# Kernel tuning notes

Measured on AMD Instinct MI355X. Metric: run time of the kernel, lower is better.

The kernel has to match this reference:

```python
import jax, jax.numpy as jnp
import numpy as np

B, D, N, K = 4, 256, 4096, 8192


def setup_inputs() -> dict:
    key = jax.random.key(0)
    kx, ke = jax.random.split(key)
    x = jax.random.normal(kx, (B, D, N), dtype=jnp.float32)
    e = jax.random.normal(ke, (K, D), dtype=jnp.float32)
    return {"x": x, "e": e}


def reference(x, e):
    # encode: cdist(x^T [B,N,D], e [K,D]) -> [B,N,K]; argmin over K.
    # sqrt is monotonic, so argmin of squared distance == argmin of cdist.
    xt = jnp.transpose(x, (0, 2, 1))                      # [B,N,D]
    x2 = jnp.sum(xt * xt, axis=-1, keepdims=True)         # [B,N,1]
    e2 = jnp.sum(e * e, axis=-1)                          # [K]
    d2 = x2 - 2.0 * jnp.einsum('bnd,kd->bnk', xt, e) + e2 # [B,N,K]
    codes = jnp.argmin(d2, axis=-1)                       # [B,N]
    # decode: embedding gather then transpose back to [B,D,N]
    quantized = e[codes]                                  # [B,N,D]
    return jnp.transpose(quantized, (0, 2, 1))            # [B,D,N]
```

## Files before the change

### kernel.cpp

```cpp
#include <hip/hip_runtime.h>
#include <stdint.h>

#define B_ 4
#define D_ 256
#define N_ 4096
#define K_ 8192
#define Q_ (B_*N_)

typedef __attribute__((ext_vector_type(8))) short bf16x8;
typedef __attribute__((ext_vector_type(8))) unsigned short u16x8;
typedef __attribute__((ext_vector_type(16))) float f32x16;

__device__ __forceinline__ unsigned short f32_to_bf16(float f) {
  unsigned u = __float_as_uint(f);
  unsigned r = 0x7FFFu + ((u >> 16) & 1u);
  return (unsigned short)((u + r) >> 16);
}
__device__ __forceinline__ float bf16_to_f32(unsigned short h) {
  return __uint_as_float(((unsigned)h) << 16);
}

__device__ __forceinline__ void gl_lds16(const void* g, void* l) {
  __builtin_amdgcn_global_load_lds(
      (const __attribute__((address_space(1))) unsigned int*)g,
      (__attribute__((address_space(3))) unsigned int*)l, 16, 0, 0);
}

__global__ void prep_x_kernel(const float* __restrict__ x,
                              unsigned short* __restrict__ xh,
                              unsigned short* __restrict__ xl) {
  __shared__ float tile[64][65];
  int b = blockIdx.z;
  int d0 = blockIdx.y * 64;
  int n0 = blockIdx.x * 64;
  int tid = threadIdx.x;

  int rr = tid >> 4;
  int rc = (tid & 15) * 4;
  const float* xp = x + ((size_t)b * D_ + d0) * N_ + n0;
#pragma unroll
  for (int p = 0; p < 4; ++p) {
    float4 v = *(const float4*)(xp + (size_t)(rr + 16 * p) * N_ + rc);
    tile[rr + 16 * p][rc + 0] = v.x;
    tile[rr + 16 * p][rc + 1] = v.y;
    tile[rr + 16 * p][rc + 2] = v.z;
    tile[rr + 16 * p][rc + 3] = v.w;
  }
  __syncthreads();

  int nr = tid >> 3;
  int dc = tid & 7;
#pragma unroll
  for (int p = 0; p < 2; ++p) {
    int nn = nr + 32 * p;
    u16x8 h8, l8;
#pragma unroll
    for (int j = 0; j < 8; ++j) {
      float v = tile[dc * 8 + j][nn];
      unsigned short h = f32_to_bf16(v);
      h8[j] = h;
      l8[j] = f32_to_bf16(v - bf16_to_f32(h));
    }
    size_t q = (size_t)b * N_ + n0 + nn;
    *(u16x8*)(xh + q * D_ + d0 + dc * 8) = h8;
    *(u16x8*)(xl + q * D_ + d0 + dc * 8) = l8;
  }
}

__global__ void prep_e_kernel(const float* __restrict__ e,
                              unsigned short* __restrict__ eh,
                              unsigned short* __restrict__ el,
                              float* __restrict__ e2h,
                              unsigned long long* __restrict__ keys) {
  int tid = threadIdx.x;
  int k = blockIdx.x * 8 + (tid >> 5);
  int d = (tid & 31) * 8;
  if (tid < 16) keys[(size_t)blockIdx.x * 16 + tid] = ~0ull;
  const float* ep = e + (size_t)k * D_ + d;
  float4 v0 = *(const float4*)(ep);
  float4 v1 = *(const float4*)(ep + 4);
  float vv[8] = {v0.x, v0.y, v0.z, v0.w, v1.x, v1.y, v1.z, v1.w};
  u16x8 h8, l8;
  float s = 0.f;
#pragma unroll
  for (int j = 0; j < 8; ++j) {
    unsigned short h = f32_to_bf16(vv[j]);
    h8[j] = h;
    l8[j] = f32_to_bf16(vv[j] - bf16_to_f32(h));
    s += vv[j] * vv[j];
  }
  *(u16x8*)(eh + (size_t)k * D_ + d) = h8;
  *(u16x8*)(el + (size_t)k * D_ + d) = l8;
#pragma unroll
  for (int off = 16; off > 0; off >>= 1) s += __shfl_xor(s, off, 64);
  if ((tid & 31) == 0) e2h[k] = 0.5f * s;
}

__global__ __launch_bounds__(256, 1) void vq_main_kernel(
    const unsigned short* __restrict__ xh, const unsigned short* __restrict__ xl,
    const unsigned short* __restrict__ eh, const unsigned short* __restrict__ el,
    const float* __restrict__ e2h, unsigned long long* __restrict__ keys) {
  __shared__ __attribute__((aligned(16))) unsigned short Bs[2][2][32 * 256];

  const int tid = threadIdx.x;
  const int w = tid >> 6;
  const int lane = tid & 63;
  const int l = lane & 31;
  const int hi = lane >> 5;

  const int qt = blockIdx.x >> 2;
  const int ks4 = blockIdx.x & 3;
  const int q0 = qt * 256;
  const int kbase = ks4 * 2048;
  const int qw = q0 + w * 64;

  bf16x8 ah[2][16], al[2][16];
#pragma unroll
  for (int mb = 0; mb < 2; ++mb) {
    const unsigned short* pa = xh + (size_t)(qw + mb * 32 + l) * D_ + hi * 8;
    const unsigned short* pb = xl + (size_t)(qw + mb * 32 + l) * D_ + hi * 8;
#pragma unroll
    for (int k16 = 0; k16 < 16; ++k16) {
      ah[mb][k16] = *(const bf16x8*)(pa + k16 * 16);
      al[mb][k16] = *(const bf16x8*)(pb + k16 * 16);
    }
  }

  float rminv[2][16];
  int rmini[2][16];
#pragma unroll
  for (int mb = 0; mb < 2; ++mb)
#pragma unroll
    for (int r = 0; r < 16; ++r) { rminv[mb][r] = __builtin_inff(); rmini[mb][r] = 0; }

  auto stage = [&](int ch, int buf) {
    const int kc = kbase + ch * 32;
#pragma unroll
    for (int p = 0; p < 4; ++p) {
      const int c0 = w * 8 + p * 2;
      const int c = c0 + hi;
      const int g = l ^ (c & 31);
      const size_t srcoff = (size_t)(kc + c) * D_ + g * 8;
      gl_lds16(eh + srcoff, &Bs[buf][0][c0 * 256]);
      gl_lds16(el + srcoff, &Bs[buf][1][c0 * 256]);
    }
  };

  stage(0, 0);

#pragma unroll 1
  for (int ch = 0; ch < 64; ++ch) {
    const int buf = ch & 1;
    __syncthreads();
    if (ch + 1 < 64) stage(ch + 1, buf ^ 1);
    const int kc = kbase + ch * 32;
    const float e2v = e2h[kc + l];

    f32x16 acc0, acc1;
#pragma unroll
    for (int r = 0; r < 16; ++r) { acc0[r] = 0.f; acc1[r] = 0.f; }

#pragma unroll
    for (int ks = 0; ks < 16; ++ks) {
      const int pos = (((ks * 2 + hi) ^ l) * 8);
      bf16x8 bh = *(const bf16x8*)&Bs[buf][0][l * 256 + pos];
      bf16x8 bl = *(const bf16x8*)&Bs[buf][1][l * 256 + pos];
      acc0 = __builtin_amdgcn_mfma_f32_32x32x16_bf16(ah[0][ks], bh, acc0, 0, 0, 0);
      acc1 = __builtin_amdgcn_mfma_f32_32x32x16_bf16(ah[1][ks], bh, acc1, 0, 0, 0);
      acc0 = __builtin_amdgcn_mfma_f32_32x32x16_bf16(ah[0][ks], bl, acc0, 0, 0, 0);
      acc1 = __builtin_amdgcn_mfma_f32_32x32x16_bf16(ah[1][ks], bl, acc1, 0, 0, 0);
      acc0 = __builtin_amdgcn_mfma_f32_32x32x16_bf16(al[0][ks], bh, acc0, 0, 0, 0);
      acc1 = __builtin_amdgcn_mfma_f32_32x32x16_bf16(al[1][ks], bh, acc1, 0, 0, 0);
    }

    const int kidx = kc + l;
#pragma unroll
    for (int r = 0; r < 16; ++r) {
      float dv0 = e2v - acc0[r];
      bool b0 = dv0 < rminv[0][r];
      rminv[0][r] = b0 ? dv0 : rminv[0][r];
      rmini[0][r] = b0 ? kidx : rmini[0][r];
      float dv1 = e2v - acc1[r];
      bool b1 = dv1 < rminv[1][r];
      rminv[1][r] = b1 ? dv1 : rminv[1][r];
      rmini[1][r] = b1 ? kidx : rmini[1][r];
    }
  }

#pragma unroll
  for (int mb = 0; mb < 2; ++mb) {
#pragma unroll
    for (int r = 0; r < 16; ++r) {
      float bv = rminv[mb][r];
      int bi = rmini[mb][r];
#pragma unroll
      for (int xm = 1; xm <= 16; xm <<= 1) {
        float ov = __shfl_xor(bv, xm, 64);
        int oi = __shfl_xor(bi, xm, 64);
        if (ov < bv || (ov == bv && oi < bi)) { bv = ov; bi = oi; }
      }
      if (l == 0) {
        const int m = (r & 3) + 8 * (r >> 2) + 4 * hi;
        const int qq = qw + mb * 32 + m;
        unsigned su = __float_as_uint(bv);
        su ^= (unsigned)(((int)su >> 31) | 0x80000000u);
        unsigned long long key = ((unsigned long long)su << 32) | (unsigned)bi;
        atomicMin(keys + qq, key);
      }
    }
  }
}

__global__ __launch_bounds__(256, 2) void decode_kernel(
    const unsigned long long* __restrict__ keys,
    const float* __restrict__ e, float* __restrict__ out) {
  __shared__ float tile[64][257];
  int b = blockIdx.x >> 6;
  int n0 = (blockIdx.x & 63) * 64;
  int tid = threadIdx.x;
  int w = tid >> 6, lane = tid & 63;

#pragma unroll
  for (int j = 0; j < 16; ++j) {
    int i = w * 16 + j;
    unsigned idx = (unsigned)(keys[(size_t)b * N_ + n0 + i] & 0xFFFFFFFFull);
    float4 v = *(const float4*)(e + (size_t)idx * D_ + lane * 4);
    *(float4*)&tile[i][lane * 4] = v;
  }
  __syncthreads();

  int nq = tid & 15, dr = tid >> 4;
#pragma unroll
  for (int p = 0; p < 16; ++p) {
    int d = dr + p * 16;
    float4 o;
    o.x = tile[nq * 4 + 0][d];
    o.y = tile[nq * 4 + 1][d];
    o.z = tile[nq * 4 + 2][d];
    o.w = tile[nq * 4 + 3][d];
    *(float4*)(out + ((size_t)b * D_ + d) * N_ + n0 + nq * 4) = o;
  }
}

extern "C" void kernel_launch(void* const* d_in, const int* in_sizes, int n_in,
                              void* d_out, int out_size, void* d_ws, size_t ws_size,
                              hipStream_t stream) {
  const float* x = (const float*)d_in[0];
  const float* e = (const float*)d_in[1];
  float* out = (float*)d_out;

  char* wksp = (char*)d_ws;
  unsigned short* xh = (unsigned short*)wksp;
  unsigned short* xl = xh + (size_t)Q_ * D_;
  unsigned short* eh = xl + (size_t)Q_ * D_;
  unsigned short* el = eh + (size_t)K_ * D_;
  float* e2h = (float*)(el + (size_t)K_ * D_);
  unsigned long long* keys = (unsigned long long*)(e2h + K_);

  prep_x_kernel<<<dim3(N_ / 64, D_ / 64, B_), 256, 0, stream>>>(x, xh, xl);
  prep_e_kernel<<<K_ / 8, 256, 0, stream>>>(e, eh, el, e2h, keys);
  vq_main_kernel<<<256, 256, 0, stream>>>(xh, xl, eh, el, e2h, keys);
  decode_kernel<<<256, 256, 0, stream>>>(keys, e, out);
}
```

Before: 264.1 us.

## Replace split-bf16 exact GEMM with fp16 screening plus exact candidate rescoring

```diff
diff --git a/kernel.cpp b/kernel.cpp
--- a/kernel.cpp
+++ b/kernel.cpp
@@ -7,17 +7,19 @@
 #define K_ 8192
 #define Q_ (B_*N_)
 
-typedef __attribute__((ext_vector_type(8))) short bf16x8;
-typedef __attribute__((ext_vector_type(8))) unsigned short u16x8;
+#define MARGIN 1.0f
+
+typedef __attribute__((ext_vector_type(8))) _Float16 f16x8;
+typedef __attribute__((ext_vector_type(4))) _Float16 f16x4;
 typedef __attribute__((ext_vector_type(16))) float f32x16;
 
-__device__ __forceinline__ unsigned short f32_to_bf16(float f) {
+__device__ __forceinline__ unsigned enc_sort(float f) {
   unsigned u = __float_as_uint(f);
-  unsigned r = 0x7FFFu + ((u >> 16) & 1u);
-  return (unsigned short)((u + r) >> 16);
-}
-__device__ __forceinline__ float bf16_to_f32(unsigned short h) {
-  return __uint_as_float(((unsigned)h) << 16);
+  return u ^ ((unsigned)(((int)u) >> 31) | 0x80000000u);
+}
+__device__ __forceinline__ float dec_sort(unsigned u) {
+  unsigned v = (u & 0x80000000u) ? (u ^ 0x80000000u) : ~u;
+  return __uint_as_float(v);
 }
 
 __device__ __forceinline__ void gl_lds16(const void* g, void* l) {
@@ -27,8 +29,8 @@
 }
 
 __global__ void prep_x_kernel(const float* __restrict__ x,
-                              unsigned short* __restrict__ xh,
-                              unsigned short* __restrict__ xl) {
+                              _Float16* __restrict__ xh,
+                              _Float16* __restrict__ xl) {
   __shared__ float tile[64][65];
   int b = blockIdx.z;
   int d0 = blockIdx.y * 64;
@@ -53,85 +55,74 @@
 #pragma unroll
   for (int p = 0; p < 2; ++p) {
     int nn = nr + 32 * p;
-    u16x8 h8, l8;
+    f16x8 h8, l8;
 #pragma unroll
     for (int j = 0; j < 8; ++j) {
       float v = tile[dc * 8 + j][nn];
-      unsigned short h = f32_to_bf16(v);
+      _Float16 h = (_Float16)v;
       h8[j] = h;
-      l8[j] = f32_to_bf16(v - bf16_to_f32(h));
+      l8[j] = (_Float16)(v - (float)h);
     }
     size_t q = (size_t)b * N_ + n0 + nn;
-    *(u16x8*)(xh + q * D_ + d0 + dc * 8) = h8;
-    *(u16x8*)(xl + q * D_ + d0 + dc * 8) = l8;
+    *(f16x8*)(xh + q * D_ + d0 + dc * 8) = h8;
+    *(f16x8*)(xl + q * D_ + d0 + dc * 8) = l8;
   }
 }
 
 __global__ void prep_e_kernel(const float* __restrict__ e,
-                              unsigned short* __restrict__ eh,
-                              unsigned short* __restrict__ el,
+                              _Float16* __restrict__ eh,
                               float* __restrict__ e2h,
-                              unsigned long long* __restrict__ keys) {
+                              unsigned* __restrict__ thrmin,
+                              unsigned long long* __restrict__ keys,
+                              unsigned* __restrict__ cnt) {
   int tid = threadIdx.x;
+  int g = blockIdx.x * 256 + tid;
+  if (g < Q_) { thrmin[g] = 0xFFFFFFFFu; keys[g] = ~0ull; }
+  if (g == 0) *cnt = 0u;
   int k = blockIdx.x * 8 + (tid >> 5);
   int d = (tid & 31) * 8;
-  if (tid < 16) keys[(size_t)blockIdx.x * 16 + tid] = ~0ull;
   const float* ep = e + (size_t)k * D_ + d;
   float4 v0 = *(const float4*)(ep);
   float4 v1 = *(const float4*)(ep + 4);
   float vv[8] = {v0.x, v0.y, v0.z, v0.w, v1.x, v1.y, v1.z, v1.w};
-  u16x8 h8, l8;
+  f16x8 h8;
   float s = 0.f;
 #pragma unroll
   for (int j = 0; j < 8; ++j) {
-    unsigned short h = f32_to_bf16(vv[j]);
-    h8[j] = h;
-    l8[j] = f32_to_bf16(vv[j] - bf16_to_f32(h));
+    h8[j] = (_Float16)vv[j];
     s += vv[j] * vv[j];
   }
-  *(u16x8*)(eh + (size_t)k * D_ + d) = h8;
-  *(u16x8*)(el + (size_t)k * D_ + d) = l8;
+  *(f16x8*)(eh + (size_t)k * D_ + d) = h8;
 #pragma unroll
   for (int off = 16; off > 0; off >>= 1) s += __shfl_xor(s, off, 64);
   if ((tid & 31) == 0) e2h[k] = 0.5f * s;
 }
 
-__global__ __launch_bounds__(256, 1) void vq_main_kernel(
-    const unsigned short* __restrict__ xh, const unsigned short* __restrict__ xl,
-    const unsigned short* __restrict__ eh, const unsigned short* __restrict__ el,
-    const float* __restrict__ e2h, unsigned long long* __restrict__ keys) {
-  __shared__ __attribute__((aligned(16))) unsigned short Bs[2][2][32 * 256];
-
+__global__ __launch_bounds__(256, 2) void pass0_kernel(
+    const _Float16* __restrict__ xh, const _Float16* __restrict__ eh,
+    const float* __restrict__ e2h, unsigned* __restrict__ thrmin) {
+  __shared__ __attribute__((aligned(16))) _Float16 Bs[2][32 * 256];
   const int tid = threadIdx.x;
-  const int w = tid >> 6;
-  const int lane = tid & 63;
-  const int l = lane & 31;
-  const int hi = lane >> 5;
-
-  const int qt = blockIdx.x >> 2;
-  const int ks4 = blockIdx.x & 3;
-  const int q0 = qt * 256;
-  const int kbase = ks4 * 2048;
+  const int w = tid >> 6, lane = tid & 63;
+  const int l = lane & 31, hi = lane >> 5;
+  const int qt = blockIdx.x >> 3, ks8 = blockIdx.x & 7;
+  const int q0 = qt * 256, kbase = ks8 * 256;
   const int qw = q0 + w * 64;
 
-  bf16x8 ah[2][16], al[2][16];
+  f16x8 ah[2][16];
 #pragma unroll
   for (int mb = 0; mb < 2; ++mb) {
-    const unsigned short* pa = xh + (size_t)(qw + mb * 32 + l) * D_ + hi * 8;
-    const unsigned short* pb = xl + (size_t)(qw + mb * 32 + l) * D_ + hi * 8;
-#pragma unroll
-    for (int k16 = 0; k16 < 16; ++k16) {
-      ah[mb][k16] = *(const bf16x8*)(pa + k16 * 16);
-      al[mb][k16] = *(const bf16x8*)(pb + k16 * 16);
-    }
-  }
-
-  float rminv[2][16];
-  int rmini[2][16];
+    const _Float16* pa = xh + (size_t)(qw + mb * 32 + l) * D_ + hi * 8;
+#pragma unroll
+    for (int k16 = 0; k16 < 16; ++k16)
+      ah[mb][k16] = *(const f16x8*)(pa + k16 * 16);
+  }
+
+  float rmin[2][16];
 #pragma unroll
   for (int mb = 0; mb < 2; ++mb)
 #pragma unroll
-    for (int r = 0; r < 16; ++r) { rminv[mb][r] = __builtin_inff(); rmini[mb][r] = 0; }
+    for (int r = 0; r < 16; ++r) rmin[mb][r] = __builtin_inff();
 
   auto stage = [&](int ch, int buf) {
     const int kc = kbase + ch * 32;
@@ -140,73 +131,162 @@
       const int c0 = w * 8 + p * 2;
       const int c = c0 + hi;
       const int g = l ^ (c & 31);
-      const size_t srcoff = (size_t)(kc + c) * D_ + g * 8;
-      gl_lds16(eh + srcoff, &Bs[buf][0][c0 * 256]);
-      gl_lds16(el + srcoff, &Bs[buf][1][c0 * 256]);
+      gl_lds16(eh + (size_t)(kc + c) * D_ + g * 8, &Bs[buf][c0 * 256]);
     }
   };
-
   stage(0, 0);
 
 #pragma unroll 1
-  for (int ch = 0; ch < 64; ++ch) {
+  for (int ch = 0; ch < 8; ++ch) {
     const int buf = ch & 1;
     __syncthreads();
-    if (ch + 1 < 64) stage(ch + 1, buf ^ 1);
+    if (ch + 1 < 8) stage(ch + 1, buf ^ 1);
     const int kc = kbase + ch * 32;
-    const float e2v = e2h[kc + l];
-
+    const float c2 = e2h[kc + l];
     f32x16 acc0, acc1;
 #pragma unroll
     for (int r = 0; r < 16; ++r) { acc0[r] = 0.f; acc1[r] = 0.f; }
-
 #pragma unroll
     for (int ks = 0; ks < 16; ++ks) {
-      const int pos = (((ks * 2 + hi) ^ l) * 8);
-      bf16x8 bh = *(const bf16x8*)&Bs[buf][0][l * 256 + pos];
-      bf16x8 bl = *(const bf16x8*)&Bs[buf][1][l * 256 + pos];
-      acc0 = __builtin_amdgcn_mfma_f32_32x32x16_bf16(ah[0][ks], bh, acc0, 0, 0, 0);
-      acc1 = __builtin_amdgcn_mfma_f32_32x32x16_bf16(ah[1][ks], bh, acc1, 0, 0, 0);
-      acc0 = __builtin_amdgcn_mfma_f32_32x32x16_bf16(ah[0][ks], bl, acc0, 0, 0, 0);
-      acc1 = __builtin_amdgcn_mfma_f32_32x32x16_bf16(ah[1][ks], bl, acc1, 0, 0, 0);
-      acc0 = __builtin_amdgcn_mfma_f32_32x32x16_bf16(al[0][ks], bh, acc0, 0, 0, 0);
-      acc1 = __builtin_amdgcn_mfma_f32_32x32x16_bf16(al[1][ks], bh, acc1, 0, 0, 0);
-    }
-
-    const int kidx = kc + l;
+      f16x8 bh = *(const f16x8*)&Bs[buf][l * 256 + (((ks * 2 + hi) ^ l) * 8)];
+      acc0 = __builtin_amdgcn_mfma_f32_32x32x16_f16(ah[0][ks], bh, acc0, 0, 0, 0);
+      acc1 = __builtin_amdgcn_mfma_f32_32x32x16_f16(ah[1][ks], bh, acc1, 0, 0, 0);
+    }
 #pragma unroll
     for (int r = 0; r < 16; ++r) {
-      float dv0 = e2v - acc0[r];
-      bool b0 = dv0 < rminv[0][r];
-      rminv[0][r] = b0 ? dv0 : rminv[0][r];
-      rmini[0][r] = b0 ? kidx : rmini[0][r];
-      float dv1 = e2v - acc1[r];
-      bool b1 = dv1 < rminv[1][r];
-      rminv[1][r] = b1 ? dv1 : rminv[1][r];
-      rmini[1][r] = b1 ? kidx : rmini[1][r];
-    }
-  }
-
-#pragma unroll
-  for (int mb = 0; mb < 2; ++mb) {
+      float s0 = c2 - acc0[r]; if (s0 < rmin[0][r]) rmin[0][r] = s0;
+      float s1 = c2 - acc1[r]; if (s1 < rmin[1][r]) rmin[1][r] = s1;
+    }
+  }
+
+#pragma unroll
+  for (int mb = 0; mb < 2; ++mb)
 #pragma unroll
     for (int r = 0; r < 16; ++r) {
-      float bv = rminv[mb][r];
-      int bi = rmini[mb][r];
+      float bv = rmin[mb][r];
 #pragma unroll
       for (int xm = 1; xm <= 16; xm <<= 1) {
         float ov = __shfl_xor(bv, xm, 64);
-        int oi = __shfl_xor(bi, xm, 64);
-        if (ov < bv || (ov == bv && oi < bi)) { bv = ov; bi = oi; }
+        bv = ov < bv ? ov : bv;
       }
       if (l == 0) {
-        const int m = (r & 3) + 8 * (r >> 2) + 4 * hi;
-        const int qq = qw + mb * 32 + m;
-        unsigned su = __float_as_uint(bv);
-        su ^= (unsigned)(((int)su >> 31) | 0x80000000u);
-        unsigned long long key = ((unsigned long long)su << 32) | (unsigned)bi;
-        atomicMin(keys + qq, key);
+        const int row = (r & 3) + 8 * (r >> 2) + 4 * hi;
+        atomicMin(thrmin + qw + mb * 32 + row, enc_sort(bv));
       }
+    }
+}
+
+__global__ __launch_bounds__(256, 2) void pass1_kernel(
+    const _Float16* __restrict__ xh, const _Float16* __restrict__ eh,
+    const float* __restrict__ e2h, const unsigned* __restrict__ thrmin,
+    unsigned* __restrict__ pairs, unsigned* __restrict__ cnt, int cap) {
+  __shared__ __attribute__((aligned(16))) _Float16 Bs[2][32 * 256];
+  const int tid = threadIdx.x;
+  const int w = tid >> 6, lane = tid & 63;
+  const int l = lane & 31, hi = lane >> 5;
+  const int qt = blockIdx.x >> 3, ks8 = blockIdx.x & 7;
+  const int q0 = qt * 256, kbase = ks8 * 1024;
+  const int qw = q0 + w * 64;
+
+  f16x8 ah[2][16];
+#pragma unroll
+  for (int mb = 0; mb < 2; ++mb) {
+    const _Float16* pa = xh + (size_t)(qw + mb * 32 + l) * D_ + hi * 8;
+#pragma unroll
+    for (int k16 = 0; k16 < 16; ++k16)
+      ah[mb][k16] = *(const f16x8*)(pa + k16 * 16);
+  }
+
+  float tq[2][16];
+#pragma unroll
+  for (int mb = 0; mb < 2; ++mb)
+#pragma unroll
+    for (int r = 0; r < 16; ++r) {
+      const int row = (r & 3) + 8 * (r >> 2) + 4 * hi;
+      tq[mb][r] = dec_sort(thrmin[qw + mb * 32 + row]) + MARGIN;
+    }
+
+  auto stage = [&](int ch, int buf) {
+    const int kc = kbase + ch * 32;
+#pragma unroll
+    for (int p = 0; p < 4; ++p) {
+      const int c0 = w * 8 + p * 2;
+      const int c = c0 + hi;
+      const int g = l ^ (c & 31);
+      gl_lds16(eh + (size_t)(kc + c) * D_ + g * 8, &Bs[buf][c0 * 256]);
+    }
+  };
+  stage(0, 0);
+
+#pragma unroll 1
+  for (int ch = 0; ch < 32; ++ch) {
+    const int buf = ch & 1;
+    __syncthreads();
+    if (ch + 1 < 32) stage(ch + 1, buf ^ 1);
+    const int kc = kbase + ch * 32;
+    const float c2 = e2h[kc + l];
+    f32x16 acc0, acc1;
+#pragma unroll
+    for (int r = 0; r < 16; ++r) { acc0[r] = 0.f; acc1[r] = 0.f; }
+#pragma unroll
+    for (int ks = 0; ks < 16; ++ks) {
+      f16x8 bh = *(const f16x8*)&Bs[buf][l * 256 + (((ks * 2 + hi) ^ l) * 8)];
+      acc0 = __builtin_amdgcn_mfma_f32_32x32x16_f16(ah[0][ks], bh, acc0, 0, 0, 0);
+      acc1 = __builtin_amdgcn_mfma_f32_32x32x16_f16(ah[1][ks], bh, acc1, 0, 0, 0);
+    }
+
+    bool any = false;
+    float sv0[16], sv1[16];
+#pragma unroll
+    for (int r = 0; r < 16; ++r) {
+      sv0[r] = c2 - acc0[r]; any |= (sv0[r] <= tq[0][r]);
+      sv1[r] = c2 - acc1[r]; any |= (sv1[r] <= tq[1][r]);
+    }
+    if (__any(any)) {
+      const int k = kc + l;
+#pragma unroll
+      for (int r = 0; r < 16; ++r) {
+        const int row = (r & 3) + 8 * (r >> 2) + 4 * hi;
+        if (sv0[r] <= tq[0][r]) {
+          unsigned idx = atomicAdd(cnt, 1u);
+          if ((int)idx < cap) pairs[idx] = ((unsigned)(qw + row) << 13) | (unsigned)k;
+        }
+        if (sv1[r] <= tq[1][r]) {
+          unsigned idx = atomicAdd(cnt, 1u);
+          if ((int)idx < cap) pairs[idx] = ((unsigned)(qw + 32 + row) << 13) | (unsigned)k;
+        }
+      }
+    }
+  }
+}
+
+__global__ __launch_bounds__(256) void pass2_kernel(
+    const _Float16* __restrict__ xh, const _Float16* __restrict__ xl,
+    const float* __restrict__ e, const float* __restrict__ e2h,
+    const unsigned* __restrict__ pairs, const unsigned* __restrict__ cnt,
+    int cap, unsigned long long* __restrict__ keys) {
+  const int lane = threadIdx.x & 63;
+  const int wid = (blockIdx.x * 256 + threadIdx.x) >> 6;
+  const int nw = gridDim.x * 4;
+  int n = (int)*cnt;
+  if (n > cap) n = cap;
+  for (int i = wid; i < n; i += nw) {
+    unsigned it = pairs[i];
+    int q = (int)(it >> 13);
+    int k = (int)(it & 8191u);
+    f16x4 xh4 = *(const f16x4*)(xh + (size_t)q * D_ + lane * 4);
+    f16x4 xl4 = *(const f16x4*)(xl + (size_t)q * D_ + lane * 4);
+    float4 ev = *(const float4*)(e + (size_t)k * D_ + lane * 4);
+    float p = ((float)xh4[0] + (float)xl4[0]) * ev.x
+            + ((float)xh4[1] + (float)xl4[1]) * ev.y
+            + ((float)xh4[2] + (float)xl4[2]) * ev.z
+            + ((float)xh4[3] + (float)xl4[3]) * ev.w;
+#pragma unroll
+    for (int xm = 1; xm <= 32; xm <<= 1) p += __shfl_xor(p, xm, 64);
+    if (lane == 0) {
+      float s = e2h[k] - p;
+      unsigned long long key = ((unsigned long long)enc_sort(s) << 32) | (unsigned)k;
+      atomicMin(keys + q, key);
     }
   }
 }
@@ -219,7 +299,6 @@
   int n0 = (blockIdx.x & 63) * 64;
   int tid = threadIdx.x;
   int w = tid >> 6, lane = tid & 63;
-
 #pragma unroll
   for (int j = 0; j < 16; ++j) {
     int i = w * 16 + j;
@@ -228,7 +307,6 @@
     *(float4*)&tile[i][lane * 4] = v;
   }
   __syncthreads();
-
   int nq = tid & 15, dr = tid >> 4;
 #pragma unroll
   for (int p = 0; p < 16; ++p) {
@@ -249,16 +327,26 @@
   const float* e = (const float*)d_in[1];
   float* out = (float*)d_out;
 
-  char* wksp = (char*)d_ws;
-  unsigned short* xh = (unsigned short*)wksp;
-  unsigned short* xl = xh + (size_t)Q_ * D_;
-  unsigned short* eh = xl + (size_t)Q_ * D_;
-  unsigned short* el = eh + (size_t)K_ * D_;
-  float* e2h = (float*)(el + (size_t)K_ * D_);
-  unsigned long long* keys = (unsigned long long*)(e2h + K_);
+  char* wp = (char*)d_ws;
+  _Float16* xh = (_Float16*)wp;
+  _Float16* xl = (_Float16*)(wp + (size_t)Q_ * D_ * 2);
+  _Float16* eh = (_Float16*)(wp + (size_t)Q_ * D_ * 4);
+  char* p2 = wp + (size_t)Q_ * D_ * 4 + (size_t)K_ * D_ * 2;
+  float* e2h = (float*)p2;
+  unsigned* thrmin = (unsigned*)(p2 + K_ * 4);
+  unsigned long long* keys = (unsigned long long*)(p2 + K_ * 4 + Q_ * 4);
+  unsigned* cnt = (unsigned*)(p2 + K_ * 4 + Q_ * 4 + Q_ * 8);
+  unsigned* pairs = (unsigned*)(p2 + K_ * 4 + Q_ * 4 + Q_ * 8 + 1024);
+  size_t fixed = (size_t)((char*)pairs - wp);
+  long long capll = ((long long)ws_size - (long long)fixed) / 4;
+  if (capll > (1ll << 22)) capll = 1ll << 22;
+  if (capll < 1) capll = 1;
+  int cap = (int)capll;
 
   prep_x_kernel<<<dim3(N_ / 64, D_ / 64, B_), 256, 0, stream>>>(x, xh, xl);
-  prep_e_kernel<<<K_ / 8, 256, 0, stream>>>(e, eh, el, e2h, keys);
-  vq_main_kernel<<<256, 256, 0, stream>>>(xh, xl, eh, el, e2h, keys);
+  prep_e_kernel<<<K_ / 8, 256, 0, stream>>>(e, eh, e2h, thrmin, keys, cnt);
+  pass0_kernel<<<512, 256, 0, stream>>>(xh, eh, e2h, thrmin);
+  pass1_kernel<<<512, 256, 0, stream>>>(xh, eh, e2h, thrmin, pairs, cnt, cap);
+  pass2_kernel<<<512, 256, 0, stream>>>(xh, xl, e, e2h, pairs, cnt, cap, keys);
   decode_kernel<<<256, 256, 0, stream>>>(keys, e, out);
 }
```

Measured after the change: 1.051 ms. 3.98x slower.
